# Kernel tuning notes

Hardware: AMD Instinct MI355X
Metric: run time of the kernel (lower is better)

## Reference

```python
import jax, jax.numpy as jnp
import numpy as np


def setup_inputs() -> dict:
    key = jax.random.key(0)
    k1, k2, k3 = jax.random.split(key, 3)
    B, Cin, H, W = 16, 128, 56, 56
    Cout, Kh, Kw = 256, 3, 3
    tensor = jax.random.normal(k1, (B, Cin, H, W), dtype=jnp.float32)
    weights = jax.random.normal(k2, (Cout, Cin, Kh, Kw), dtype=jnp.float32) * 0.05
    bias = jax.random.normal(k3, (Cout,), dtype=jnp.float32) * 0.05
    return {"tensor": tensor, "weights": weights, "bias": bias}


def reference(tensor, weights, bias):
    # OpticalConvolution: unfold (im2col) -> per-output-channel augmented dot
    # products (w . patch + b). Mathematically this is a standard 2D conv with
    # bias, expressed here as one fused conv instead of a per-channel loop.
    stride, padding, dilation = (1, 1), ((1, 1), (1, 1)), (1, 1)
    out = jax.lax.conv_general_dilated(
        tensor, weights,
        window_strides=stride,
        padding=padding,
        rhs_dilation=dilation,
        dimension_numbers=("NCHW", "OIHW", "NCHW"),
    )
    return out + bias[None, :, None, None]  # [B, Cout, H_out, W_out]
```

## Files before the change

### kernel.cpp

```cpp
#include <hip/hip_runtime.h>
#include <hip/hip_bf16.h>

typedef unsigned short ushort_t;
typedef unsigned int uint_t;

#define CIN   128
#define COUT  256
#define HH    56
#define WW    56
#define HWSZ  3136
#define BATCH 16
#define NPIX  50176
#define KTOT  1152

typedef __attribute__((ext_vector_type(8))) short bf16x8;
typedef __attribute__((ext_vector_type(4))) float f32x4;

__device__ __forceinline__ ushort_t f2bf(float v) {
    union { float f; uint_t u; } c; c.f = v;
    uint_t u = c.u;
    u += 0x7FFFu + ((u >> 16) & 1u);
    return (ushort_t)(u >> 16);
}

__device__ __forceinline__ uint_t pk2bf(float lo, float hi) {
    __hip_bfloat162 h = __float22bfloat162_rn(make_float2(lo, hi));
    union { __hip_bfloat162 h; uint_t u; } c; c.h = h;
    return c.u;
}

__global__ __launch_bounds__(256) void prep(
    const float* __restrict__ tensor, const float* __restrict__ weights,
    ushort_t* __restrict__ Ib, ushort_t* __restrict__ Wt, ushort_t* __restrict__ guard)
{
    __shared__ __align__(16) uint_t lds_u[64 * 68];
    const int tid = threadIdx.x;

    if (blockIdx.x < 784) {
        int t   = blockIdx.x;
        int b   = t / 49;
        int hwt = t - b * 49;
        int hw0 = hwt * 64;
        const float* src = tensor + (size_t)b * CIN * HWSZ + hw0;
        #pragma unroll
        for (int k = 0; k < 4; ++k) {
            int t2 = tid + k * 256;
            int hb = t2 & 15;
            int cp = t2 >> 4;
            const float* s0 = src + (size_t)(2 * cp) * HWSZ + hb * 4;
            float4 a  = *(const float4*)s0;
            float4 bb = *(const float4*)(s0 + HWSZ);
            uint_t w0 = pk2bf(a.x, bb.x);
            uint_t w1 = pk2bf(a.y, bb.y);
            uint_t w2 = pk2bf(a.z, bb.z);
            uint_t w3 = pk2bf(a.w, bb.w);
            int c16  = cp >> 2;
            int lb   = cp & 3;
            int c16p = c16 ^ (hb & 7);
            uint_t* base = &lds_u[(hb * 4) * 68 + c16p * 4 + lb];
            base[0 * 68] = w0;
            base[1 * 68] = w1;
            base[2 * 68] = w2;
            base[3 * 68] = w3;
        }
        __syncthreads();
        ushort_t* dst = Ib + ((size_t)b * HWSZ + hw0) * CIN;
        #pragma unroll
        for (int k = 0; k < 4; ++k) {
            int s2  = tid + k * 256;
            int ho  = s2 >> 4;
            int c16 = s2 & 15;
            int c16p = c16 ^ ((ho >> 2) & 7);
            uint4 v = *(const uint4*)&lds_u[ho * 68 + c16p * 4];
            *(uint4*)(dst + ho * 128 + c16 * 8) = v;
        }
    } else {
        int co = blockIdx.x - 784;
        ushort_t* lds_s = (ushort_t*)lds_u;
        const float* src = weights + (size_t)co * KTOT;
        #pragma unroll
        for (int k = 0; k < 5; ++k) {
            int idx = tid + k * 256;
            if (idx < KTOT) {
                int ci  = idx / 9;
                int pos = idx - ci * 9;
                lds_s[pos * 128 + ci] = f2bf(src[idx]);
            }
        }
        __syncthreads();
        ushort_t* dst = Wt + (size_t)co * KTOT;
        #pragma unroll
        for (int k = 0; k < 5; ++k) {
            int idx = tid + k * 256;
            if (idx < KTOT) dst[idx] = lds_s[idx];
        }
        if (blockIdx.x == 784 && tid < 128) ((uint_t*)guard)[tid] = 0;
    }
}

__global__ __launch_bounds__(256) void conv_gemm(
    const ushort_t* __restrict__ Wt,
    const ushort_t* __restrict__ Ib,
    const float* __restrict__ bias,
    float* __restrict__ out,
    const ushort_t* __restrict__ guard)
{
    __shared__ ushort_t A_lds[2][128 * 32];
    __shared__ ushort_t B_lds[2][128 * 32];

    const int tid  = threadIdx.x;
    const int wave = tid >> 6;
    const int lane = tid & 63;
    const int quad = lane >> 4;
    const int l16  = lane & 15;

    const int g  = blockIdx.x >> 4;
    const int bm = (blockIdx.x >> 3) & 1;
    const int bn = g * 8 + (blockIdx.x & 7);

    const int wm = (wave >> 1) * 64;
    const int wn = (wave & 1) * 64;

    const ushort_t* aCh[2];
    const ushort_t* pbCh[2];
    int py[2], px[2];
    #pragma unroll
    for (int q = 0; q < 2; ++q) {
        int slot = wave * 128 + q * 64 + lane;
        int r  = slot >> 2;
        int c  = slot & 3;
        int cF = c ^ ((r >> 1) & 3);
        aCh[q] = Wt + (size_t)(bm * 128 + r) * KTOT + cF * 8;
        int pix = bn * 128 + r;
        int b_  = pix / HWSZ;
        int rem = pix - b_ * HWSZ;
        int y_  = rem / WW;
        int x_  = rem - y_ * WW;
        py[q] = y_; px[q] = x_;
        pbCh[q] = Ib + (size_t)pix * CIN + cF * 8;
    }
    const int ldsOff = (wave * 128) * 8;
    const int xorc   = (l16 >> 1) & 3;

    const ushort_t* bSel[9][2];
    #pragma unroll
    for (int pos = 0; pos < 9; ++pos) {
        const int dy = pos / 3 - 1;
        const int dx = pos % 3 - 1;
        #pragma unroll
        for (int q = 0; q < 2; ++q) {
            int yy = py[q] + dy, xx = px[q] + dx;
            bool ok = ((uint_t)yy < (uint_t)HH) && ((uint_t)xx < (uint_t)WW);
            bSel[pos][q] = ok ? (pbCh[q] + (dy * WW + dx) * CIN) : guard;
        }
    }

    const f32x4 zero = {0.f, 0.f, 0.f, 0.f};
    f32x4 acc[4][4];
    #pragma unroll
    for (int i = 0; i < 4; ++i)
        #pragma unroll
        for (int j = 0; j < 4; ++j) acc[i][j] = zero;

    auto stage = [&](int s, int buf) {
        const int pos = s >> 2;
        const int cc  = s & 3;
        #pragma unroll
        for (int q = 0; q < 2; ++q) {
            __builtin_amdgcn_global_load_lds(
                (const __attribute__((address_space(1))) void*)(aCh[q] + s * 32),
                (__attribute__((address_space(3))) void*)(&A_lds[buf][ldsOff + q * 512]),
                16, 0, 0);
            __builtin_amdgcn_global_load_lds(
                (const __attribute__((address_space(1))) void*)(bSel[pos][q] + cc * 32),
                (__attribute__((address_space(3))) void*)(&B_lds[buf][ldsOff + q * 512]),
                16, 0, 0);
        }
    };

    stage(0, 0);
    #pragma unroll
    for (int s = 0; s < 36; ++s) {
        __syncthreads();
        if (s < 35) stage(s + 1, (s + 1) & 1);
        const int p = s & 1;
        bf16x8 af[4], bfr[4];
        #pragma unroll
        for (int i = 0; i < 4; ++i)
            af[i] = *(const bf16x8*)&A_lds[p][(wm + i * 16 + l16) * 32 + (quad ^ xorc) * 8];
        #pragma unroll
        for (int j = 0; j < 4; ++j)
            bfr[j] = *(const bf16x8*)&B_lds[p][(wn + j * 16 + l16) * 32 + (quad ^ xorc) * 8];
        #pragma unroll
        for (int i = 0; i < 4; ++i)
            #pragma unroll
            for (int j = 0; j < 4; ++j)
                acc[i][j] = __builtin_amdgcn_mfma_f32_16x16x32_bf16(
                    af[i], bfr[j], acc[i][j], 0, 0, 0);
    }

    int obase[4];
    #pragma unroll
    for (int j = 0; j < 4; ++j) {
        int pix = bn * 128 + wn + j * 16 + l16;
        int b_  = pix / HWSZ;
        int rem = pix - b_ * HWSZ;
        obase[j] = b_ * (COUT * HWSZ) + rem;
    }
    #pragma unroll
    for (int i = 0; i < 4; ++i) {
        #pragma unroll
        for (int r = 0; r < 4; ++r) {
            int co = bm * 128 + wm + i * 16 + quad * 4 + r;
            float bv = bias[co];
            int coOff = co * HWSZ;
            #pragma unroll
            for (int j = 0; j < 4; ++j) {
                out[(size_t)(obase[j] + coOff)] = acc[i][j][r] + bv;
            }
        }
    }
}

__global__ void naive_conv(const float* __restrict__ in, const float* __restrict__ w,
                           const float* __restrict__ bias, float* __restrict__ out, int total) {
    int idx = blockIdx.x * 256 + threadIdx.x;
    if (idx >= total) return;
    int x = idx % WW; int t = idx / WW;
    int y = t % HH; t /= HH;
    int co = t % COUT; int b = t / COUT;
    float s = bias[co];
    const float* wr = w + (size_t)co * KTOT;
    for (int ci = 0; ci < CIN; ++ci) {
        const float* ir = in + (size_t)(b * CIN + ci) * HWSZ;
        for (int kh = 0; kh < 3; ++kh) {
            int yy = y + kh - 1;
            if ((uint_t)yy >= (uint_t)HH) continue;
            for (int kw = 0; kw < 3; ++kw) {
                int xx = x + kw - 1;
                if ((uint_t)xx >= (uint_t)WW) continue;
                s += ir[yy * WW + xx] * wr[ci * 9 + kh * 3 + kw];
            }
        }
    }
    out[idx] = s;
}

extern "C" void kernel_launch(void* const* d_in, const int* in_sizes, int n_in,
                              void* d_out, int out_size, void* d_ws, size_t ws_size,
                              hipStream_t stream) {
    const float* tensor  = (const float*)d_in[0];
    const float* weights = (const float*)d_in[1];
    const float* bias    = (const float*)d_in[2];
    float* out = (float*)d_out;

    const size_t GUARD    = 1024;
    const size_t WT_BYTES = (size_t)COUT * KTOT * 2;
    const size_t IB_BYTES = (size_t)NPIX * CIN * 2;
    const size_t NEED     = GUARD + WT_BYTES + IB_BYTES;

    if (ws_size >= NEED) {
        ushort_t* guard = (ushort_t*)d_ws;
        ushort_t* Wt    = (ushort_t*)((char*)d_ws + GUARD);
        ushort_t* Ib    = (ushort_t*)((char*)d_ws + GUARD + WT_BYTES);
        prep<<<784 + COUT, 256, 0, stream>>>(tensor, weights, Ib, Wt, guard);
        conv_gemm<<<(COUT / 128) * (NPIX / 128), 256, 0, stream>>>(Wt, Ib, bias, out, guard);
    } else {
        int total = BATCH * COUT * HWSZ;
        naive_conv<<<(total + 255) / 256, 256, 0, stream>>>(tensor, weights, bias, out, total);
    }
}
```

Baseline: 125.8 us.

## Prepack weights into MFMA fragment layout and load A directly to registers

The prep kernel now writes bf16 weights in a layout that matches the MFMA A-fragment order, so each lane can load its A operand straight from global memory into registers. This removes A staging in shared memory. The GEMM block changes to 128 threads with a 128x64 output tile: each wave owns 64 output channels and both waves share a 64-pixel B tile in LDS. The grid doubles and the launch bounds allow 3 blocks per CU. The trade-off is that A is no longer shared between waves through LDS, so global/L2 traffic for weights goes up, while LDS usage and sync cost per block go down.

```diff
diff --git a/kernel.cpp b/kernel.cpp
--- a/kernel.cpp
+++ b/kernel.cpp
@@ -31,7 +31,7 @@
 
 __global__ __launch_bounds__(256) void prep(
     const float* __restrict__ tensor, const float* __restrict__ weights,
-    ushort_t* __restrict__ Ib, ushort_t* __restrict__ Wt, ushort_t* __restrict__ guard)
+    ushort_t* __restrict__ Ib, ushort_t* __restrict__ A2, ushort_t* __restrict__ guard)
 {
     __shared__ __align__(16) uint_t lds_u[64 * 68];
     const int tid = threadIdx.x;
@@ -88,25 +88,27 @@
             }
         }
         __syncthreads();
-        ushort_t* dst = Wt + (size_t)co * KTOT;
-        #pragma unroll
-        for (int k = 0; k < 5; ++k) {
-            int idx = tid + k * 256;
-            if (idx < KTOT) dst[idx] = lds_s[idx];
+        int mt  = co >> 6;
+        int ii  = (co >> 4) & 3;
+        int l16 = co & 15;
+        if (tid < 144) {
+            int s    = tid >> 2;
+            int quad = tid & 3;
+            uint4 v = *(const uint4*)&lds_s[(s >> 2) * 128 + (s & 3) * 32 + quad * 8];
+            *(uint4*)(A2 + ((size_t)((mt * 36 + s) * 4 + ii) * 64 + quad * 16 + l16) * 8) = v;
         }
         if (blockIdx.x == 784 && tid < 128) ((uint_t*)guard)[tid] = 0;
     }
 }
 
-__global__ __launch_bounds__(256) void conv_gemm(
-    const ushort_t* __restrict__ Wt,
+__global__ __launch_bounds__(128, 3) void conv_gemm(
+    const ushort_t* __restrict__ A2,
     const ushort_t* __restrict__ Ib,
     const float* __restrict__ bias,
     float* __restrict__ out,
     const ushort_t* __restrict__ guard)
 {
-    __shared__ ushort_t A_lds[2][128 * 32];
-    __shared__ ushort_t B_lds[2][128 * 32];
+    __shared__ ushort_t B_lds[2][64 * 32];
 
     const int tid  = threadIdx.x;
     const int wave = tid >> 6;
@@ -117,43 +119,46 @@
     const int g  = blockIdx.x >> 4;
     const int bm = (blockIdx.x >> 3) & 1;
     const int bn = g * 8 + (blockIdx.x & 7);
-
-    const int wm = (wave >> 1) * 64;
-    const int wn = (wave & 1) * 64;
-
-    const ushort_t* aCh[2];
-    const ushort_t* pbCh[2];
-    int py[2], px[2];
-    #pragma unroll
-    for (int q = 0; q < 2; ++q) {
-        int slot = wave * 128 + q * 64 + lane;
+    const int mt = bm * 2 + wave;
+
+    int bOff[9][2];
+    #pragma unroll
+    for (int k = 0; k < 2; ++k) {
+        int slot = k * 128 + tid;
         int r  = slot >> 2;
         int c  = slot & 3;
         int cF = c ^ ((r >> 1) & 3);
-        aCh[q] = Wt + (size_t)(bm * 128 + r) * KTOT + cF * 8;
-        int pix = bn * 128 + r;
+        int pix = bn * 64 + r;
         int b_  = pix / HWSZ;
         int rem = pix - b_ * HWSZ;
         int y_  = rem / WW;
         int x_  = rem - y_ * WW;
-        py[q] = y_; px[q] = x_;
-        pbCh[q] = Ib + (size_t)pix * CIN + cF * 8;
-    }
-    const int ldsOff = (wave * 128) * 8;
-    const int xorc   = (l16 >> 1) & 3;
-
-    const ushort_t* bSel[9][2];
-    #pragma unroll
-    for (int pos = 0; pos < 9; ++pos) {
-        const int dy = pos / 3 - 1;
-        const int dx = pos % 3 - 1;
-        #pragma unroll
-        for (int q = 0; q < 2; ++q) {
-            int yy = py[q] + dy, xx = px[q] + dx;
+        int base = pix * CIN + cF * 8;
+        int goff = (int)(guard - Ib);
+        #pragma unroll
+        for (int pos = 0; pos < 9; ++pos) {
+            const int dy = pos / 3 - 1;
+            const int dx = pos % 3 - 1;
+            int yy = y_ + dy, xx = x_ + dx;
             bool ok = ((uint_t)yy < (uint_t)HH) && ((uint_t)xx < (uint_t)WW);
-            bSel[pos][q] = ok ? (pbCh[q] + (dy * WW + dx) * CIN) : guard;
-        }
-    }
+            bOff[pos][k] = ok ? (base + (dy * WW + dx) * CIN) : goff;
+        }
+    }
+    const int xorc = (l16 >> 1) & 3;
+
+    const ushort_t* aBase = A2 + ((size_t)mt * 36 * 4 * 64 + lane) * 8;
+
+    auto stageB = [&](int s, int buf) {
+        const int pos = s >> 2;
+        const int cc  = s & 3;
+        #pragma unroll
+        for (int k = 0; k < 2; ++k) {
+            __builtin_amdgcn_global_load_lds(
+                (const __attribute__((address_space(1))) void*)(Ib + bOff[pos][k] + cc * 32),
+                (__attribute__((address_space(3))) void*)(&B_lds[buf][(k * 128 + wave * 64) * 8]),
+                16, 0, 0);
+        }
+    };
 
     const f32x4 zero = {0.f, 0.f, 0.f, 0.f};
     f32x4 acc[4][4];
@@ -162,47 +167,40 @@
         #pragma unroll
         for (int j = 0; j < 4; ++j) acc[i][j] = zero;
 
-    auto stage = [&](int s, int buf) {
-        const int pos = s >> 2;
-        const int cc  = s & 3;
-        #pragma unroll
-        for (int q = 0; q < 2; ++q) {
-            __builtin_amdgcn_global_load_lds(
-                (const __attribute__((address_space(1))) void*)(aCh[q] + s * 32),
-                (__attribute__((address_space(3))) void*)(&A_lds[buf][ldsOff + q * 512]),
-                16, 0, 0);
-            __builtin_amdgcn_global_load_lds(
-                (const __attribute__((address_space(1))) void*)(bSel[pos][q] + cc * 32),
-                (__attribute__((address_space(3))) void*)(&B_lds[buf][ldsOff + q * 512]),
-                16, 0, 0);
-        }
-    };
-
-    stage(0, 0);
+    bf16x8 aCur[4], aNxt[4];
+    stageB(0, 0);
+    #pragma unroll
+    for (int i = 0; i < 4; ++i)
+        aCur[i] = *(const bf16x8*)(aBase + (size_t)i * 512);
+
     #pragma unroll
     for (int s = 0; s < 36; ++s) {
         __syncthreads();
-        if (s < 35) stage(s + 1, (s + 1) & 1);
+        if (s < 35) {
+            stageB(s + 1, (s + 1) & 1);
+            #pragma unroll
+            for (int i = 0; i < 4; ++i)
+                aNxt[i] = *(const bf16x8*)(aBase + (size_t)((s + 1) * 4 + i) * 512);
+        }
         const int p = s & 1;
-        bf16x8 af[4], bfr[4];
-        #pragma unroll
-        for (int i = 0; i < 4; ++i)
-            af[i] = *(const bf16x8*)&A_lds[p][(wm + i * 16 + l16) * 32 + (quad ^ xorc) * 8];
+        bf16x8 bfr[4];
         #pragma unroll
         for (int j = 0; j < 4; ++j)
-            bfr[j] = *(const bf16x8*)&B_lds[p][(wn + j * 16 + l16) * 32 + (quad ^ xorc) * 8];
+            bfr[j] = *(const bf16x8*)&B_lds[p][(j * 16 + l16) * 32 + (quad ^ xorc) * 8];
         #pragma unroll
         for (int i = 0; i < 4; ++i)
             #pragma unroll
             for (int j = 0; j < 4; ++j)
                 acc[i][j] = __builtin_amdgcn_mfma_f32_16x16x32_bf16(
-                    af[i], bfr[j], acc[i][j], 0, 0, 0);
+                    aCur[i], bfr[j], acc[i][j], 0, 0, 0);
+        #pragma unroll
+        for (int i = 0; i < 4; ++i) aCur[i] = aNxt[i];
     }
 
     int obase[4];
     #pragma unroll
     for (int j = 0; j < 4; ++j) {
-        int pix = bn * 128 + wn + j * 16 + l16;
+        int pix = bn * 64 + j * 16 + l16;
         int b_  = pix / HWSZ;
         int rem = pix - b_ * HWSZ;
         obase[j] = b_ * (COUT * HWSZ) + rem;
@@ -211,7 +209,7 @@
     for (int i = 0; i < 4; ++i) {
         #pragma unroll
         for (int r = 0; r < 4; ++r) {
-            int co = bm * 128 + wm + i * 16 + quad * 4 + r;
+            int co = bm * 128 + wave * 64 + i * 16 + quad * 4 + r;
             float bv = bias[co];
             int coOff = co * HWSZ;
             #pragma unroll
@@ -255,16 +253,16 @@
     float* out = (float*)d_out;
 
     const size_t GUARD    = 1024;
-    const size_t WT_BYTES = (size_t)COUT * KTOT * 2;
+    const size_t A2_BYTES = (size_t)COUT * KTOT * 2;
     const size_t IB_BYTES = (size_t)NPIX * CIN * 2;
-    const size_t NEED     = GUARD + WT_BYTES + IB_BYTES;
+    const size_t NEED     = GUARD + A2_BYTES + IB_BYTES;
 
     if (ws_size >= NEED) {
         ushort_t* guard = (ushort_t*)d_ws;
-        ushort_t* Wt    = (ushort_t*)((char*)d_ws + GUARD);
-        ushort_t* Ib    = (ushort_t*)((char*)d_ws + GUARD + WT_BYTES);
-        prep<<<784 + COUT, 256, 0, stream>>>(tensor, weights, Ib, Wt, guard);
-        conv_gemm<<<(COUT / 128) * (NPIX / 128), 256, 0, stream>>>(Wt, Ib, bias, out, guard);
+        ushort_t* A2    = (ushort_t*)((char*)d_ws + GUARD);
+        ushort_t* Ib    = (ushort_t*)((char*)d_ws + GUARD + A2_BYTES);
+        prep<<<784 + COUT, 256, 0, stream>>>(tensor, weights, Ib, A2, guard);
+        conv_gemm<<<2 * 784, 128, 0, stream>>>(A2, Ib, bias, out, guard);
     } else {
         int total = BATCH * COUT * HWSZ;
         naive_conv<<<(total + 255) / 256, 256, 0, stream>>>(tensor, weights, bias, out, total);
```

Measured after the change: 129.9 us. 3.3% more time.
